# Optimization experiments

Measured on AMD Instinct MI355X. Metric: run time of the kernel, lower is better.

The kernel has to match this reference:

```python
import jax, jax.numpy as jnp
import numpy as np

D = 512      # model_size
NH = 8       # num_heads
HD = D // NH # head_dim = 64
T = 2048     # seq len (qlen == klen == pos len)
B = 2        # batch

# flattened Bayesian parameter layout (matches flatten_list order in the module)
_SHAPES = [(3 * D, D), (D, D), (D, D), (3 * D,), (D,), (D,), (NH, HD), (NH, HD)]
_N = sum(int(np.prod(s)) for s in _SHAPES)  # 1,314,304


def _unflatten(w):
    out, i = [], 0
    for s in _SHAPES:
        n = int(np.prod(s))
        out.append(w[i:i + n].reshape(s))
        i += n
    return out


def _rel_shift(x):
    # Transformer-XL relative shift: x is [qlen, klen, B, NH]
    q, k, b, n = x.shape
    x = jnp.pad(x, ((0, 0), (1, 0), (0, 0), (0, 0)))  # zero col at front of klen axis
    x = x.reshape(k + 1, q, b, n)[1:]
    return x.reshape(q, k, b, n)


def setup_inputs() -> dict:
    key = jax.random.key(0)
    k1, k2, k3, k4, k5 = jax.random.split(key, 5)
    inp = jax.random.normal(k1, (T, B, D), dtype=jnp.float32)
    pos = jax.random.normal(k2, (T, 1, D), dtype=jnp.float32)
    std = np.sqrt(2.0 / (D + D))
    mu = jax.random.normal(k3, (_N,), dtype=jnp.float32) * std
    rho = -5.0 + 0.1 * jax.random.normal(k4, (_N,), dtype=jnp.float32)
    eps = jax.random.normal(k5, (_N,), dtype=jnp.float32)
    attn_mask = jnp.triu(jnp.ones((T, T), dtype=bool), 1)  # True = masked (future)
    return {"input": inp, "pos": pos, "attn_mask": attn_mask,
            "mu": mu, "rho": rho, "eps": eps}


def reference(input, pos, attn_mask, mu, rho, eps):
    # Gaussian reparameterized weight sample: w = mu + softplus(rho) * eps
    w = mu + jax.nn.softplus(rho) * eps
    (in_w, out_w, pos_w, in_b, out_b, pos_b, r_w_bias, r_r_bias) = _unflatten(w)

    # input projection -> q, k, v : [T, B, NH, HD]
    qkv = input @ in_w.T + in_b                      # [T, B, 3D]
    q, k, v = jnp.split(qkv, 3, axis=-1)
    q = q.reshape(T, B, NH, HD)
    k = k.reshape(T, B, NH, HD)
    v = v.reshape(T, B, NH, HD)

    # relative position projection: [R, NH, HD]
    r = (pos[:, 0, :] @ pos_w.T + pos_b).reshape(-1, NH, HD)

    # content score (AC) and position score (BD) with rel-shift
    AC = jnp.einsum('ibnd,jbnd->ijbn', q + r_w_bias, k)
    BD = _rel_shift(jnp.einsum('ibnd,jnd->ijbn', q + r_r_bias, r))

    scale = np.float32(1.0 / np.sqrt(HD))
    score = (AC + BD) * scale                        # [T, T, B, NH]
    score = jnp.where(attn_mask[:, :, None, None],
                      jnp.finfo(score.dtype).min, score)
    probs = jax.nn.softmax(score, axis=1)

    attn_vec = jnp.einsum('ijbn,jbnd->ibnd', probs, v).reshape(T, B, D)
    return attn_vec @ out_w.T + out_b                # [T, B, D]
```

## Files before the change

### kernel.cpp

```cpp
#include <hip/hip_runtime.h>


typedef float f32x4 __attribute__((ext_vector_type(4)));
typedef short bf16x8 __attribute__((ext_vector_type(8)));

#define NW 1314304
#define OFF_INB  1310720
#define OFF_INW  0
#define OFF_OUTW 786432
#define OFF_POSW 1048576
#define BB_IN  0
#define BB_OUT 1536
#define BB_POS 2048
#define BB_RW  2560
#define BB_RR  3072

#define L2E 1.44269504088896340736f

__device__ __forceinline__ unsigned short f2bf(float x) {
  unsigned u = __builtin_bit_cast(unsigned, x);
  u += 0x7fffu + ((u >> 16) & 1u);
  return (unsigned short)(u >> 16);
}
__device__ __forceinline__ float bf2f(unsigned short s) {
  return __builtin_bit_cast(float, ((unsigned)s) << 16);
}
__device__ __forceinline__ unsigned pk2(float lo, float hi) {
  return (unsigned)f2bf(lo) | ((unsigned)f2bf(hi) << 16);
}

__global__ void prep_kernel(const float* __restrict__ mu, const float* __restrict__ rho,
                            const float* __restrict__ eps,
                            const float* __restrict__ input, const float* __restrict__ pos,
                            unsigned short* __restrict__ Wh, float* __restrict__ Bf,
                            unsigned short* __restrict__ inH, unsigned short* __restrict__ posH) {
  const int bx = blockIdx.x;
  if (bx < 1284) {
    int i = (bx * 256 + threadIdx.x) * 4;
    if (i < NW) {
      float4 m = *(const float4*)&mu[i];
      float4 r = *(const float4*)&rho[i];
      float4 e = *(const float4*)&eps[i];
      float w0 = m.x + ((r.x > 20.f) ? r.x : log1pf(expf(r.x))) * e.x;
      float w1 = m.y + ((r.y > 20.f) ? r.y : log1pf(expf(r.y))) * e.y;
      float w2 = m.z + ((r.z > 20.f) ? r.z : log1pf(expf(r.z))) * e.z;
      float w3 = m.w + ((r.w > 20.f) ? r.w : log1pf(expf(r.w))) * e.w;
      union { unsigned short s[4]; uint2 u; } p;
      p.s[0] = f2bf(w0); p.s[1] = f2bf(w1); p.s[2] = f2bf(w2); p.s[3] = f2bf(w3);
      *(uint2*)&Wh[i] = p.u;
      if (i >= OFF_INB) {
        float4 b; b.x = w0; b.y = w1; b.z = w2; b.w = w3;
        *(float4*)&Bf[i - OFF_INB] = b;
      }
    }
  } else if (bx < 3332) {
    int i = ((bx - 1284) * 256 + threadIdx.x) * 4;
    float4 v = *(const float4*)&input[i];
    union { unsigned short s[4]; uint2 u; } p;
    p.s[0] = f2bf(v.x); p.s[1] = f2bf(v.y); p.s[2] = f2bf(v.z); p.s[3] = f2bf(v.w);
    *(uint2*)&inH[i] = p.u;
  } else {
    int i = ((bx - 3332) * 256 + threadIdx.x) * 4;
    float4 v = *(const float4*)&pos[i];
    union { unsigned short s[4]; uint2 u; } p;
    p.s[0] = f2bf(v.x); p.s[1] = f2bf(v.y); p.s[2] = f2bf(v.z); p.s[3] = f2bf(v.w);
    *(uint2*)&posH[i] = p.u;
  }
}

__device__ __forceinline__ void gemm128_loop(const unsigned short* __restrict__ A,
                                             const unsigned short* __restrict__ B,
                                             unsigned short* As, unsigned short* Bs,
                                             f32x4 (&acc)[4][4]) {
  const int tid = threadIdx.x;
  const int wv = tid >> 6, lane = tid & 63, g = lane >> 4, cc = lane & 15;
  const int wr = wv >> 1, wc = wv & 1;
  const int row = tid >> 1, half = tid & 1;
  const unsigned short* Ap = A + (size_t)row * 512 + 32 * half;
  const unsigned short* Bp = B + (size_t)row * 512 + 32 * half;
  const int lb = row * 72 + 32 * half;

#pragma unroll
  for (int j = 0; j < 4; j++) {
    *(uint4*)&As[lb + 8 * j] = *(const uint4*)(Ap + 8 * j);
    *(uint4*)&Bs[lb + 8 * j] = *(const uint4*)(Bp + 8 * j);
  }
  __syncthreads();

  for (int it = 0; it < 8; it++) {
    uint4 pa[4], pb[4];
    const bool pf = (it < 7);
    if (pf) {
      const unsigned short* An = Ap + 64 * (it + 1);
      const unsigned short* Bn = Bp + 64 * (it + 1);
#pragma unroll
      for (int j = 0; j < 4; j++) {
        pa[j] = *(const uint4*)(An + 8 * j);
        pb[j] = *(const uint4*)(Bn + 8 * j);
      }
    }
    __builtin_amdgcn_s_setprio(1);
#pragma unroll
    for (int ks = 0; ks < 2; ks++) {
      bf16x8 af[4], bf[4];
#pragma unroll
      for (int fm = 0; fm < 4; fm++)
        af[fm] = *(const bf16x8*)&As[(64 * wr + 16 * fm + cc) * 72 + 32 * ks + 8 * g];
#pragma unroll
      for (int fn = 0; fn < 4; fn++)
        bf[fn] = *(const bf16x8*)&Bs[(64 * wc + 16 * fn + cc) * 72 + 32 * ks + 8 * g];
#pragma unroll
      for (int fm = 0; fm < 4; fm++)
#pragma unroll
        for (int fn = 0; fn < 4; fn++)
          acc[fm][fn] = __builtin_amdgcn_mfma_f32_16x16x32_bf16(af[fm], bf[fn], acc[fm][fn], 0, 0, 0);
    }
    __builtin_amdgcn_s_setprio(0);
    __syncthreads();
    if (pf) {
#pragma unroll
      for (int j = 0; j < 4; j++) {
        *(uint4*)&As[lb + 8 * j] = pa[j];
        *(uint4*)&Bs[lb + 8 * j] = pb[j];
      }
    }
    __syncthreads();
  }
}

__global__ __launch_bounds__(256, 2)
void gemm01_kernel(const unsigned short* __restrict__ inH, const unsigned short* __restrict__ posH,
                   const unsigned short* __restrict__ Wh, const float* __restrict__ Bf,
                   unsigned short* __restrict__ qrw, unsigned short* __restrict__ qrr,
                   unsigned short* __restrict__ kbuf, unsigned short* __restrict__ vT,
                   unsigned short* __restrict__ rbuf) {
  __shared__ __align__(16) unsigned short As[128 * 72];
  __shared__ __align__(16) unsigned short Bs[128 * 72];
  const int bx = blockIdx.x;
  const int tid = threadIdx.x;
  const int wv = tid >> 6, lane = tid & 63, g = lane >> 4, cc = lane & 15;
  const int wr = wv >> 1, wc = wv & 1;

  const bool isR = (bx >= 384);
  int m0, n0;
  const unsigned short *A, *W;
  if (!isR) {
    m0 = (bx & 31) << 7; n0 = (bx >> 5) << 7;
    A = inH + (size_t)m0 * 512;  W = Wh + OFF_INW + (size_t)n0 * 512;
  } else {
    const int t = bx - 384;
    m0 = (t & 15) << 7; n0 = (t >> 4) << 7;
    A = posH + (size_t)m0 * 512; W = Wh + OFF_POSW + (size_t)n0 * 512;
  }

  f32x4 acc[4][4];
#pragma unroll
  for (int i = 0; i < 4; i++)
#pragma unroll
    for (int j = 0; j < 4; j++) { acc[i][j][0] = 0.f; acc[i][j][1] = 0.f; acc[i][j][2] = 0.f; acc[i][j][3] = 0.f; }
  gemm128_loop(A, W, As, Bs, acc);

  const int sec = isR ? 3 : (n0 >> 9);
  const int t0 = m0 >> 1;

#pragma unroll
  for (int h = 0; h < 2; h++) {
    const int nh2 = ((n0 + 64 * h) >> 6) & 7;
    if (sec == 0) {
      if (wc == h) {
#pragma unroll
        for (int fn = 0; fn < 4; fn++) {
          const int colg = n0 + 64 * h + 16 * fn + cc;
          const float b0 = Bf[BB_IN + colg];
          const float brw = Bf[BB_RW + colg], brr = Bf[BB_RR + colg];
#pragma unroll
          for (int fm = 0; fm < 4; fm++)
#pragma unroll
            for (int r = 0; r < 4; r++) {
              const int ml = 64 * wr + 16 * fm + 4 * g + r;
              As[ml * 72 + 16 * fn + cc] = f2bf((acc[fm][fn][r] + b0 + brw) * 0.125f);
              Bs[ml * 72 + 16 * fn + cc] = f2bf((acc[fm][fn][r] + b0 + brr) * 0.125f);
            }
        }
      }
      __syncthreads();
      for (int c = tid; c < 1024; c += 256) {
        const int ml = c >> 3, hc = c & 7;
        const int bb2 = ml & 1, tl = ml >> 1;
        uint4 v1 = *(const uint4*)&As[ml * 72 + 8 * hc];
        uint4 v2 = *(const uint4*)&Bs[ml * 72 + 8 * hc];
        const size_t dst = ((size_t)(bb2 * 8 + nh2) * 2048 + t0 + tl) * 64 + 8 * hc;
        *(uint4*)&qrw[dst] = v1;
        *(uint4*)&qrr[dst] = v2;
      }
      __syncthreads();
    } else if (sec == 1) {
      if (wc == h) {
#pragma unroll
        for (int fn = 0; fn < 4; fn++) {
          const float b0 = Bf[BB_IN + n0 + 64 * h + 16 * fn + cc];
#pragma unroll
          for (int fm = 0; fm < 4; fm++)
#pragma unroll
            for (int r = 0; r < 4; r++)
              As[(64 * wr + 16 * fm + 4 * g + r) * 72 + 16 * fn + cc] = f2bf(acc[fm][fn][r] + b0);
        }
      }
      __syncthreads();
      for (int c = tid; c < 1024; c += 256) {
        const int ml = c >> 3, hc = c & 7;
        const int bb2 = ml & 1, tl = ml >> 1;
        uint4 v1 = *(const uint4*)&As[ml * 72 + 8 * hc];
        *(uint4*)&kbuf[((size_t)(bb2 * 8 + nh2) * 2048 + t0 + tl) * 64 + 8 * hc] = v1;
      }
      __syncthreads();
    } else if (sec == 2) {
      if (wc == h) {
#pragma unroll
        for (int fn = 0; fn < 4; fn++) {
          const float b0 = Bf[BB_IN + n0 + 64 * h + 16 * fn + cc];
#pragma unroll
          for (int fm = 0; fm < 4; fm++)
#pragma unroll
            for (int r = 0; r < 4; r++)
              As[(64 * wr + 16 * fm + 4 * g + r) * 72 + 16 * fn + cc] = f2bf(acc[fm][fn][r] + b0);
        }
      }
      __syncthreads();
      for (int c = tid; c < 1024; c += 256) {
        const int ncol = c >> 4;
        const int rem = c & 15, bb2 = rem >> 3, jc = rem & 7;
        union { unsigned short s[8]; uint4 u; } pk;
#pragma unroll
        for (int jt = 0; jt < 8; jt++)
          pk.s[jt] = As[(2 * (8 * jc + jt) + bb2) * 72 + ncol];
        *(uint4*)&vT[((size_t)(bb2 * 8 + nh2) * 64 + ncol) * 2048 + t0 + 8 * jc] = pk.u;
      }
      __syncthreads();
    } else {
      if (wc == h) {
#pragma unroll
        for (int fn = 0; fn < 4; fn++) {
          const float b0 = Bf[BB_POS + n0 + 64 * h + 16 * fn + cc];
#pragma unroll
          for (int fm = 0; fm < 4; fm++)
#pragma unroll
            for (int r = 0; r < 4; r++)
              As[(64 * wr + 16 * fm + 4 * g + r) * 72 + 16 * fn + cc] = f2bf(acc[fm][fn][r] + b0);
        }
      }
      __syncthreads();
      for (int c = tid; c < 1024; c += 256) {
        const int ml = c >> 3, hc = c & 7;
        uint4 v1 = *(const uint4*)&As[ml * 72 + 8 * hc];
        *(uint4*)&rbuf[((size_t)nh2 * 2048 + m0 + ml) * 64 + 8 * hc] = v1;
      }
      __syncthreads();
    }
  }
}

__global__ __launch_bounds__(256, 2)
void gemmO_kernel(const unsigned short* __restrict__ av, const unsigned short* __restrict__ W,
                  const float* __restrict__ Bf, float* __restrict__ outp) {
  __shared__ __align__(16) unsigned short As[128 * 72];
  __shared__ __align__(16) unsigned short Bs[128 * 72];
  const int bx = blockIdx.x;
  const int tid = threadIdx.x;
  const int wv = tid >> 6, lane = tid & 63, g = lane >> 4, cc = lane & 15;
  const int wr = wv >> 1, wc = wv & 1;
  const int m0 = (bx & 31) << 7, n0 = (bx >> 5) << 7;

  f32x4 acc[4][4];
#pragma unroll
  for (int i = 0; i < 4; i++)
#pragma unroll
    for (int j = 0; j < 4; j++) { acc[i][j][0] = 0.f; acc[i][j][1] = 0.f; acc[i][j][2] = 0.f; acc[i][j][3] = 0.f; }
  gemm128_loop(av + (size_t)m0 * 512, W + (size_t)n0 * 512, As, Bs, acc);

#pragma unroll
  for (int fn = 0; fn < 4; fn++) {
    const int col = n0 + 64 * wc + 16 * fn + cc;
    const float b0 = Bf[BB_OUT + col];
#pragma unroll
    for (int fm = 0; fm < 4; fm++)
#pragma unroll
      for (int r = 0; r < 4; r++) {
        const int mrow = m0 + 64 * wr + 16 * fm + 4 * g + r;
        outp[(size_t)mrow * 512 + col] = acc[fm][fn][r] + b0;
      }
  }
}

__global__ __launch_bounds__(256, 3)
void attn_kernel(const unsigned short* __restrict__ qrw, const unsigned short* __restrict__ qrr,
                 const unsigned short* __restrict__ kb, const unsigned short* __restrict__ vt,
                 const unsigned short* __restrict__ rb, unsigned short* __restrict__ av,
                 unsigned short* __restrict__ pO, float* __restrict__ pStats)
{
  __shared__ __align__(16) unsigned short Ks[64 * 72];
  __shared__ __align__(16) unsigned short Vs[64 * 72];
  __shared__ __align__(16) unsigned short Rs[128 * 72];
  __shared__ __align__(16) unsigned short GPs[4 * 16 * 84];

  const int tid = threadIdx.x;
  const int wv = tid >> 6, lane = tid & 63, g = lane >> 4, cc = lane & 15;
  const int bx = (int)blockIdx.x;
  const int bn = bx & 15;
  const int sid = 79 - (bx >> 4);
  int qt, s, ns;
  if (sid < 8)       { qt = sid;                s = 0;           ns = 1; }
  else if (sid < 24) { qt = 8 + ((sid - 8) >> 1); s = (sid - 8) & 1; ns = 2; }
  else if (sid < 48) { const int t = sid - 24; const int q3 = t / 3; qt = 16 + q3; s = t - 3 * q3; ns = 3; }
  else               { const int t = sid - 48; qt = 24 + (t >> 2); s = t & 3; ns = 4; }
  const int kt0 = s * 8;
  const int kt1 = (kt0 + 8 < qt + 1) ? (kt0 + 8) : (qt + 1);

  const int nh = bn & 7, bb = bn >> 3;
  const int i0 = qt * 64;
  const int i0g = i0 + wv * 16;
  const int w0base = 1984 - i0;

  const size_t qko = (size_t)bn * 2048 * 64;
  const size_t ro = (size_t)nh * 2048 * 64;

  bf16x8 qw[2], qr[2];
#pragma unroll
  for (int ks = 0; ks < 2; ks++) {
    qw[ks] = *(const bf16x8*)&qrw[qko + (size_t)(i0g + cc) * 64 + 32 * ks + 8 * g];
    qr[ks] = *(const bf16x8*)&qrr[qko + (size_t)(i0g + cc) * 64 + 32 * ks + 8 * g];
  }

  float m_run = -3.0e38f, l_run = 0.f;
  f32x4 o[4];
#pragma unroll
  for (int i = 0; i < 4; i++) { o[i][0] = 0.f; o[i][1] = 0.f; o[i][2] = 0.f; o[i][3] = 0.f; }

  const int srow = tid >> 2, sq = tid & 3;
  const int rrow = tid >> 1, rhalf = tid & 1;
  unsigned short* Gw = &GPs[wv * 1344];
  const int rbase = 48 - 16 * wv;

  {
    const unsigned short* kp = &kb[qko + (size_t)(kt0 * 64 + srow) * 64 + 16 * sq];
    *(uint4*)&Ks[srow * 72 + 16 * sq]     = *(const uint4*)kp;
    *(uint4*)&Ks[srow * 72 + 16 * sq + 8] = *(const uint4*)(kp + 8);
    const unsigned short* vp = &vt[qko + (size_t)srow * 2048 + kt0 * 64 + 16 * sq];
    *(uint4*)&Vs[srow * 72 + 16 * sq]     = *(const uint4*)vp;
    *(uint4*)&Vs[srow * 72 + 16 * sq + 8] = *(const uint4*)(vp + 8);
    const int u0 = w0base + kt0 * 64 + rrow;
    const int uc0 = u0 > 2047 ? 2047 : u0;
    const unsigned short* rp = &rb[ro + (size_t)uc0 * 64 + 32 * rhalf];
    unsigned short* rd = &Rs[(u0 & 127) * 72 + 32 * rhalf];
    *(uint4*)rd        = *(const uint4*)rp;
    *(uint4*)(rd + 8)  = *(const uint4*)(rp + 8);
    *(uint4*)(rd + 16) = *(const uint4*)(rp + 16);
    *(uint4*)(rd + 24) = *(const uint4*)(rp + 24);
  }
  __syncthreads();

  for (int kt = kt0; kt < kt1; kt++) {
    const int j0 = kt * 64;
    const int w0k = w0base + j0;
    const bool pf = (kt + 1 < kt1);

    uint4 ka0, ka1, va0, va1, ra0, ra1;
    int rslot = 0;
    if (pf) {
      const unsigned short* kp = &kb[qko + (size_t)(j0 + 64 + srow) * 64 + 16 * sq];
      ka0 = *(const uint4*)kp; ka1 = *(const uint4*)(kp + 8);
      const unsigned short* vp = &vt[qko + (size_t)srow * 2048 + j0 + 64 + 16 * sq];
      va0 = *(const uint4*)vp; va1 = *(const uint4*)(vp + 8);
      const int unew = w0k + 128 + (tid >> 2);
      rslot = unew & 127;
      const int uc = unew > 2047 ? 2047 : unew;
      const unsigned short* rp = &rb[ro + (size_t)uc * 64 + 16 * sq];
      ra0 = *(const uint4*)rp; ra1 = *(const uint4*)(rp + 8);
    }

    f32x4 st[4];
#pragma unroll
    for (int i = 0; i < 4; i++) { st[i][0] = 0.f; st[i][1] = 0.f; st[i][2] = 0.f; st[i][3] = 0.f; }
    __builtin_amdgcn_s_setprio(1);
#pragma unroll
    for (int ks = 0; ks < 2; ks++) {
#pragma unroll
      for (int fm = 0; fm < 4; fm++) {
        bf16x8 ka = *(const bf16x8*)&Ks[(16 * fm + cc) * 72 + 32 * ks + 8 * g];
        st[fm] = __builtin_amdgcn_mfma_f32_16x16x32_bf16(ka, qw[ks], st[fm], 0, 0, 0);
      }
    }
    f32x4 gt[5];
#pragma unroll
    for (int i = 0; i < 5; i++) { gt[i][0] = 0.f; gt[i][1] = 0.f; gt[i][2] = 0.f; gt[i][3] = 0.f; }
    const int rr0 = w0k + rbase + cc;
#pragma unroll
    for (int ks = 0; ks < 2; ks++) {
#pragma unroll
      for (int fm = 0; fm < 5; fm++) {
        const int rrw = (rr0 + 16 * fm) & 127;
        bf16x8 ra = *(const bf16x8*)&Rs[rrw * 72 + 32 * ks + 8 * g];
        gt[fm] = __builtin_amdgcn_mfma_f32_16x16x32_bf16(ra, qr[ks], gt[fm], 0, 0, 0);
      }
    }
    __builtin_amdgcn_s_setprio(0);

#pragma unroll
    for (int fm = 0; fm < 5; fm++) {
      uint2 w;
      w.x = pk2(gt[fm][0], gt[fm][1]);
      w.y = pk2(gt[fm][2], gt[fm][3]);
      *(uint2*)&Gw[cc * 84 + 16 * fm + 4 * g] = w;
    }

    float p[4][4];
    float tm = -3.0e38f;
    const bool diag = (kt == qt);
    const int c00 = 15 - cc + 4 * g;
#pragma unroll
    for (int fm = 0; fm < 4; fm++) {
      const int c0 = c00 + 16 * fm;
      const int e0 = c0 & ~1;
      const unsigned short* gp = &Gw[cc * 84 + e0];
      unsigned d0 = *(const unsigned*)gp;
      unsigned d1 = *(const unsigned*)(gp + 2);
      unsigned d2 = *(const unsigned*)(gp + 4);
      unsigned lo01, lo23;
      if (c0 & 1) { lo01 = (d0 >> 16) | (d1 << 16); lo23 = (d1 >> 16) | (d2 << 16); }
      else        { lo01 = d0; lo23 = d1; }
      float bd0 = bf2f((unsigned short)(lo01 & 0xffffu));
      float bd1 = bf2f((unsigned short)(lo01 >> 16));
      float bd2 = bf2f((unsigned short)(lo23 & 0xffffu));
      float bd3 = bf2f((unsigned short)(lo23 >> 16));
      float sv0 = st[fm][0] + bd0;
      float sv1 = st[fm][1] + bd1;
      float sv2 = st[fm][2] + bd2;
      float sv3 = st[fm][3] + bd3;
      if (diag) {
        const int jj = 16 * fm + 4 * g;
        const int lim = cc + 16 * wv;
        if (jj + 0 > lim) sv0 = -3.0e38f;
        if (jj + 1 > lim) sv1 = -3.0e38f;
        if (jj + 2 > lim) sv2 = -3.0e38f;
        if (jj + 3 > lim) sv3 = -3.0e38f;
      }
      p[fm][0] = sv0; p[fm][1] = sv1; p[fm][2] = sv2; p[fm][3] = sv3;
      tm = fmaxf(tm, fmaxf(fmaxf(sv0, sv1), fmaxf(sv2, sv3)));
    }
    tm = fmaxf(tm, __shfl_xor(tm, 16));
    tm = fmaxf(tm, __shfl_xor(tm, 32));
    const bool defer = __all(tm - m_run <= 8.0f);
    const float m_new = defer ? m_run : fmaxf(m_run, tm);
    float sc = 1.0f;
    if (!defer) sc = exp2f((m_run - m_new) * L2E);
    float ps = 0.f;
#pragma unroll
    for (int fm = 0; fm < 4; fm++)
#pragma unroll
      for (int r = 0; r < 4; r++) {
        float pv = exp2f((p[fm][r] - m_new) * L2E);
        p[fm][r] = pv;
        ps += pv;
      }
    ps += __shfl_xor(ps, 16);
    ps += __shfl_xor(ps, 32);
    l_run = l_run * sc + ps;
    m_run = m_new;

    if (!defer) {
      float scr[4];
#pragma unroll
      for (int r = 0; r < 4; r++) scr[r] = __shfl(sc, 4 * g + r);
#pragma unroll
      for (int fn = 0; fn < 4; fn++)
#pragma unroll
        for (int r = 0; r < 4; r++) o[fn][r] *= scr[r];
    }

#pragma unroll
    for (int fm = 0; fm < 4; fm++) {
      uint2 w;
      w.x = pk2(p[fm][0], p[fm][1]);
      w.y = pk2(p[fm][2], p[fm][3]);
      *(uint2*)&Gw[cc * 72 + 16 * fm + 4 * g] = w;
    }
    bf16x8 pa[2];
#pragma unroll
    for (int ks = 0; ks < 2; ks++)
      pa[ks] = *(const bf16x8*)&Gw[cc * 72 + 32 * ks + 8 * g];

    __builtin_amdgcn_s_setprio(1);
#pragma unroll
    for (int ks = 0; ks < 2; ks++) {
#pragma unroll
      for (int fn = 0; fn < 4; fn++) {
        bf16x8 vb = *(const bf16x8*)&Vs[(16 * fn + cc) * 72 + 32 * ks + 8 * g];
        o[fn] = __builtin_amdgcn_mfma_f32_16x16x32_bf16(pa[ks], vb, o[fn], 0, 0, 0);
      }
    }
    __builtin_amdgcn_s_setprio(0);

    __syncthreads();
    if (pf) {
      *(uint4*)&Ks[srow * 72 + 16 * sq]     = ka0;
      *(uint4*)&Ks[srow * 72 + 16 * sq + 8] = ka1;
      *(uint4*)&Vs[srow * 72 + 16 * sq]     = va0;
      *(uint4*)&Vs[srow * 72 + 16 * sq + 8] = va1;
      unsigned short* rd = &Rs[rslot * 72 + 16 * sq];
      *(uint4*)rd       = ra0;
      *(uint4*)(rd + 8) = ra1;
    }
    __syncthreads();
  }

  if (ns == 1) {
    const float inv = 1.0f / l_run;
    float invr[4];
#pragma unroll
    for (int r = 0; r < 4; r++) invr[r] = __shfl(inv, 4 * g + r);
#pragma unroll
    for (int fn = 0; fn < 4; fn++) {
      const int hd = 16 * fn + cc;
#pragma unroll
      for (int r = 0; r < 4; r++) {
        const int irow = i0g + 4 * g + r;
        av[((size_t)(irow * 2 + bb) * 8 + nh) * 64 + hd] = f2bf(o[fn][r] * invr[r]);
      }
    }
  } else {
    const size_t slot = (size_t)(bn * 80 + sid);
#pragma unroll
    for (int fn = 0; fn < 4; fn++) {
      const int hd = 16 * fn + cc;
#pragma unroll
      for (int r = 0; r < 4; r++)
        pO[slot * 4096 + (16 * wv + 4 * g + r) * 64 + hd] = f2bf(o[fn][r]);
    }
    if (g == 0) {
      pStats[slot * 128 + (16 * wv + cc) * 2]     = m_run;
      pStats[slot * 128 + (16 * wv + cc) * 2 + 1] = l_run;
    }
  }
}

__global__ __launch_bounds__(256)
void combine_kernel(const unsigned short* __restrict__ pO, const float* __restrict__ pStats,
                    unsigned short* __restrict__ av) {
  const int bxx = (int)blockIdx.x;
  const int bn = bxx & 15, qt = 8 + (bxx >> 4);
  const int nh = bn & 7, bb = bn >> 3;
  const int ns = (qt >> 3) + 1;
  const int sid0 = (qt < 16) ? (8 + (qt - 8) * 2)
                 : (qt < 24) ? (24 + (qt - 16) * 3)
                             : (48 + (qt - 24) * 4);
  const int tid = threadIdx.x;
  const int ql = tid >> 2, hq = tid & 3;
  const size_t sb = (size_t)(bn * 80 + sid0);

  float M = -3.0e38f;
  for (int i = 0; i < ns; i++)
    M = fmaxf(M, pStats[(sb + i) * 128 + ql * 2]);

  float L = 0.f;
  float accv[16];
#pragma unroll
  for (int j = 0; j < 16; j++) accv[j] = 0.f;
  for (int i = 0; i < ns; i++) {
    const float mi = pStats[(sb + i) * 128 + ql * 2];
    const float li = pStats[(sb + i) * 128 + ql * 2 + 1];
    const float w = exp2f((mi - M) * L2E);
    L += w * li;
    union { uint4 u; unsigned short s[8]; } c0, c1;
    const unsigned short* src = &pO[(sb + i) * 4096 + ql * 64 + 16 * hq];
    c0.u = *(const uint4*)src;
    c1.u = *(const uint4*)(src + 8);
#pragma unroll
    for (int j = 0; j < 8; j++) accv[j]     += w * bf2f(c0.s[j]);
#pragma unroll
    for (int j = 0; j < 8; j++) accv[8 + j] += w * bf2f(c1.s[j]);
  }
  const float inv = 1.0f / L;
  union { uint4 u; unsigned short s[8]; } o0, o1;
#pragma unroll
  for (int j = 0; j < 8; j++) o0.s[j] = f2bf(accv[j] * inv);
#pragma unroll
  for (int j = 0; j < 8; j++) o1.s[j] = f2bf(accv[8 + j] * inv);
  const int q = qt * 64 + ql;
  unsigned short* dst = &av[((size_t)(q * 2 + bb) * 8 + nh) * 64 + 16 * hq];
  *(uint4*)dst       = o0.u;
  *(uint4*)(dst + 8) = o1.u;
}

extern "C" void kernel_launch(void* const* d_in, const int* in_sizes, int n_in,
                              void* d_out, int out_size, void* d_ws, size_t ws_size,
                              hipStream_t stream) {
  const float* input = (const float*)d_in[0];
  const float* pos   = (const float*)d_in[1];
  const float* mu  = (const float*)d_in[3];
  const float* rho = (const float*)d_in[4];
  const float* eps = (const float*)d_in[5];
  float* out = (float*)d_out;

  char* ws = (char*)d_ws;
  unsigned short* Wh   = (unsigned short*)ws;
  float*          Bf   = (float*)(ws + 2628608);
  unsigned short* inH  = (unsigned short*)(ws + 2642944);
  unsigned short* posH = (unsigned short*)(ws + 6837248);
  unsigned short* qrw  = (unsigned short*)(ws + 8934400);
  unsigned short* qrr  = (unsigned short*)(ws + 13128704);
  unsigned short* kbuf = (unsigned short*)(ws + 17323008);
  unsigned short* vT   = (unsigned short*)(ws + 21517312);
  unsigned short* rbuf = (unsigned short*)(ws + 25711616);
  unsigned short* pO   = (unsigned short*)(ws + 27808768);
  float*          pSt  = (float*)(ws + 38294528);
  unsigned short* av   = inH;

  prep_kernel<<<dim3(4356), dim3(256), 0, stream>>>(mu, rho, eps, input, pos, Wh, Bf, inH, posH);
  gemm01_kernel<<<dim3(448), dim3(256), 0, stream>>>(inH, posH, Wh, Bf, qrw, qrr, kbuf, vT, rbuf);
  attn_kernel<<<dim3(1280), dim3(256), 0, stream>>>(qrw, qrr, kbuf, vT, rbuf, av, pO, pSt);
  combine_kernel<<<dim3(384), dim3(256), 0, stream>>>(pO, pSt, av);
  gemmO_kernel<<<dim3(128), dim3(256), 0, stream>>>(av, Wh + OFF_OUTW, Bf, out);
}
```

Baseline: 211.7 us.

## Halve GEMM tile width to 128x64 to double block counts; drop lazy softmax rescale

The QKV/pos and output projection GEMMs now use 128x64 output tiles instead of 128x128. Each wave computes a 32x64 slice, and the grids grow from 448 to 896 and from 128 to 256 blocks, which should fill the many CUs better. In the attention kernel, the deferred-max trick that skipped the rescale when the max grew by at most 8 is removed, so the output is rescaled on every tile. That removes a wave vote and a branch but adds shuffles and multiplies on every iteration, while the smaller GEMM tiles give less operand reuse.

```diff
diff --git a/kernel.cpp b/kernel.cpp
--- a/kernel.cpp
+++ b/kernel.cpp
@@ -68,66 +68,6 @@
   }
 }
 
-__device__ __forceinline__ void gemm128_loop(const unsigned short* __restrict__ A,
-                                             const unsigned short* __restrict__ B,
-                                             unsigned short* As, unsigned short* Bs,
-                                             f32x4 (&acc)[4][4]) {
-  const int tid = threadIdx.x;
-  const int wv = tid >> 6, lane = tid & 63, g = lane >> 4, cc = lane & 15;
-  const int wr = wv >> 1, wc = wv & 1;
-  const int row = tid >> 1, half = tid & 1;
-  const unsigned short* Ap = A + (size_t)row * 512 + 32 * half;
-  const unsigned short* Bp = B + (size_t)row * 512 + 32 * half;
-  const int lb = row * 72 + 32 * half;
-
-#pragma unroll
-  for (int j = 0; j < 4; j++) {
-    *(uint4*)&As[lb + 8 * j] = *(const uint4*)(Ap + 8 * j);
-    *(uint4*)&Bs[lb + 8 * j] = *(const uint4*)(Bp + 8 * j);
-  }
-  __syncthreads();
-
-  for (int it = 0; it < 8; it++) {
-    uint4 pa[4], pb[4];
-    const bool pf = (it < 7);
-    if (pf) {
-      const unsigned short* An = Ap + 64 * (it + 1);
-      const unsigned short* Bn = Bp + 64 * (it + 1);
-#pragma unroll
-      for (int j = 0; j < 4; j++) {
-        pa[j] = *(const uint4*)(An + 8 * j);
-        pb[j] = *(const uint4*)(Bn + 8 * j);
-      }
-    }
-    __builtin_amdgcn_s_setprio(1);
-#pragma unroll
-    for (int ks = 0; ks < 2; ks++) {
-      bf16x8 af[4], bf[4];
-#pragma unroll
-      for (int fm = 0; fm < 4; fm++)
-        af[fm] = *(const bf16x8*)&As[(64 * wr + 16 * fm + cc) * 72 + 32 * ks + 8 * g];
-#pragma unroll
-      for (int fn = 0; fn < 4; fn++)
-        bf[fn] = *(const bf16x8*)&Bs[(64 * wc + 16 * fn + cc) * 72 + 32 * ks + 8 * g];
-#pragma unroll
-      for (int fm = 0; fm < 4; fm++)
-#pragma unroll
-        for (int fn = 0; fn < 4; fn++)
-          acc[fm][fn] = __builtin_amdgcn_mfma_f32_16x16x32_bf16(af[fm], bf[fn], acc[fm][fn], 0, 0, 0);
-    }
-    __builtin_amdgcn_s_setprio(0);
-    __syncthreads();
-    if (pf) {
-#pragma unroll
-      for (int j = 0; j < 4; j++) {
-        *(uint4*)&As[lb + 8 * j] = pa[j];
-        *(uint4*)&Bs[lb + 8 * j] = pb[j];
-      }
-    }
-    __syncthreads();
-  }
-}
-
 __global__ __launch_bounds__(256, 2)
 void gemm01_kernel(const unsigned short* __restrict__ inH, const unsigned short* __restrict__ posH,
                    const unsigned short* __restrict__ Wh, const float* __restrict__ Bf,
@@ -139,123 +79,153 @@
   const int bx = blockIdx.x;
   const int tid = threadIdx.x;
   const int wv = tid >> 6, lane = tid & 63, g = lane >> 4, cc = lane & 15;
-  const int wr = wv >> 1, wc = wv & 1;
-
-  const bool isR = (bx >= 384);
+
+  const bool isR = (bx >= 768);
   int m0, n0;
   const unsigned short *A, *W;
   if (!isR) {
-    m0 = (bx & 31) << 7; n0 = (bx >> 5) << 7;
+    m0 = (bx & 31) << 7; n0 = (bx >> 5) << 6;
     A = inH + (size_t)m0 * 512;  W = Wh + OFF_INW + (size_t)n0 * 512;
   } else {
-    const int t = bx - 384;
-    m0 = (t & 15) << 7; n0 = (t >> 4) << 7;
+    const int t = bx - 768;
+    m0 = (t & 15) << 7; n0 = (t >> 4) << 6;
     A = posH + (size_t)m0 * 512; W = Wh + OFF_POSW + (size_t)n0 * 512;
   }
 
-  f32x4 acc[4][4];
-#pragma unroll
-  for (int i = 0; i < 4; i++)
-#pragma unroll
-    for (int j = 0; j < 4; j++) { acc[i][j][0] = 0.f; acc[i][j][1] = 0.f; acc[i][j][2] = 0.f; acc[i][j][3] = 0.f; }
-  gemm128_loop(A, W, As, Bs, acc);
-
+  const int row2 = tid >> 1, h2 = tid & 1;
+  const int row4 = tid >> 2, q4 = tid & 3;
+  const unsigned short* Ap = A + (size_t)row2 * 512 + 32 * h2;
+  const unsigned short* Bp = W + (size_t)row4 * 512 + 16 * q4;
+  const int lba = row2 * 72 + 32 * h2;
+  const int lbb = row4 * 72 + 16 * q4;
+
+  f32x4 acc[2][4] = {};
+
+#pragma unroll
+  for (int j = 0; j < 4; j++) *(uint4*)&As[lba + 8 * j] = *(const uint4*)(Ap + 8 * j);
+#pragma unroll
+  for (int j = 0; j < 2; j++) *(uint4*)&Bs[lbb + 8 * j] = *(const uint4*)(Bp + 8 * j);
+  __syncthreads();
+
+  for (int it = 0; it < 8; it++) {
+    uint4 pa[4], pb[2];
+    const bool pf = (it < 7);
+    if (pf) {
+      const unsigned short* An = Ap + 64 * (it + 1);
+      const unsigned short* Bn = Bp + 64 * (it + 1);
+#pragma unroll
+      for (int j = 0; j < 4; j++) pa[j] = *(const uint4*)(An + 8 * j);
+#pragma unroll
+      for (int j = 0; j < 2; j++) pb[j] = *(const uint4*)(Bn + 8 * j);
+    }
+    __builtin_amdgcn_s_setprio(1);
+#pragma unroll
+    for (int ks = 0; ks < 2; ks++) {
+      bf16x8 af[2], bf[4];
+#pragma unroll
+      for (int fm = 0; fm < 2; fm++)
+        af[fm] = *(const bf16x8*)&As[(32 * wv + 16 * fm + cc) * 72 + 32 * ks + 8 * g];
+#pragma unroll
+      for (int fn = 0; fn < 4; fn++)
+        bf[fn] = *(const bf16x8*)&Bs[(16 * fn + cc) * 72 + 32 * ks + 8 * g];
+#pragma unroll
+      for (int fm = 0; fm < 2; fm++)
+#pragma unroll
+        for (int fn = 0; fn < 4; fn++)
+          acc[fm][fn] = __builtin_amdgcn_mfma_f32_16x16x32_bf16(af[fm], bf[fn], acc[fm][fn], 0, 0, 0);
+    }
+    __builtin_amdgcn_s_setprio(0);
+    __syncthreads();
+    if (pf) {
+#pragma unroll
+      for (int j = 0; j < 4; j++) *(uint4*)&As[lba + 8 * j] = pa[j];
+#pragma unroll
+      for (int j = 0; j < 2; j++) *(uint4*)&Bs[lbb + 8 * j] = pb[j];
+    }
+    __syncthreads();
+  }
+
+  const int nh2 = (n0 >> 6) & 7;
   const int sec = isR ? 3 : (n0 >> 9);
   const int t0 = m0 >> 1;
 
-#pragma unroll
-  for (int h = 0; h < 2; h++) {
-    const int nh2 = ((n0 + 64 * h) >> 6) & 7;
-    if (sec == 0) {
-      if (wc == h) {
-#pragma unroll
-        for (int fn = 0; fn < 4; fn++) {
-          const int colg = n0 + 64 * h + 16 * fn + cc;
-          const float b0 = Bf[BB_IN + colg];
-          const float brw = Bf[BB_RW + colg], brr = Bf[BB_RR + colg];
-#pragma unroll
-          for (int fm = 0; fm < 4; fm++)
-#pragma unroll
-            for (int r = 0; r < 4; r++) {
-              const int ml = 64 * wr + 16 * fm + 4 * g + r;
-              As[ml * 72 + 16 * fn + cc] = f2bf((acc[fm][fn][r] + b0 + brw) * 0.125f);
-              Bs[ml * 72 + 16 * fn + cc] = f2bf((acc[fm][fn][r] + b0 + brr) * 0.125f);
-            }
+  if (sec == 0) {
+#pragma unroll
+    for (int fn = 0; fn < 4; fn++) {
+      const int colg = n0 + 16 * fn + cc;
+      const float b0 = Bf[BB_IN + colg];
+      const float brw = Bf[BB_RW + colg], brr = Bf[BB_RR + colg];
+#pragma unroll
+      for (int fm = 0; fm < 2; fm++)
+#pragma unroll
+        for (int r = 0; r < 4; r++) {
+          const int ml = 32 * wv + 16 * fm + 4 * g + r;
+          As[ml * 72 + 16 * fn + cc] = f2bf((acc[fm][fn][r] + b0 + brw) * 0.125f);
+          Bs[ml * 72 + 16 * fn + cc] = f2bf((acc[fm][fn][r] + b0 + brr) * 0.125f);
         }
-      }
-      __syncthreads();
-      for (int c = tid; c < 1024; c += 256) {
-        const int ml = c >> 3, hc = c & 7;
-        const int bb2 = ml & 1, tl = ml >> 1;
-        uint4 v1 = *(const uint4*)&As[ml * 72 + 8 * hc];
-        uint4 v2 = *(const uint4*)&Bs[ml * 72 + 8 * hc];
-        const size_t dst = ((size_t)(bb2 * 8 + nh2) * 2048 + t0 + tl) * 64 + 8 * hc;
-        *(uint4*)&qrw[dst] = v1;
-        *(uint4*)&qrr[dst] = v2;
-      }
-      __syncthreads();
-    } else if (sec == 1) {
-      if (wc == h) {
-#pragma unroll
-        for (int fn = 0; fn < 4; fn++) {
-          const float b0 = Bf[BB_IN + n0 + 64 * h + 16 * fn + cc];
-#pragma unroll
-          for (int fm = 0; fm < 4; fm++)
-#pragma unroll
-            for (int r = 0; r < 4; r++)
-              As[(64 * wr + 16 * fm + 4 * g + r) * 72 + 16 * fn + cc] = f2bf(acc[fm][fn][r] + b0);
-        }
-      }
-      __syncthreads();
-      for (int c = tid; c < 1024; c += 256) {
-        const int ml = c >> 3, hc = c & 7;
-        const int bb2 = ml & 1, tl = ml >> 1;
-        uint4 v1 = *(const uint4*)&As[ml * 72 + 8 * hc];
-        *(uint4*)&kbuf[((size_t)(bb2 * 8 + nh2) * 2048 + t0 + tl) * 64 + 8 * hc] = v1;
-      }
-      __syncthreads();
-    } else if (sec == 2) {
-      if (wc == h) {
-#pragma unroll
-        for (int fn = 0; fn < 4; fn++) {
-          const float b0 = Bf[BB_IN + n0 + 64 * h + 16 * fn + cc];
-#pragma unroll
-          for (int fm = 0; fm < 4; fm++)
-#pragma unroll
-            for (int r = 0; r < 4; r++)
-              As[(64 * wr + 16 * fm + 4 * g + r) * 72 + 16 * fn + cc] = f2bf(acc[fm][fn][r] + b0);
-        }
-      }
-      __syncthreads();
-      for (int c = tid; c < 1024; c += 256) {
-        const int ncol = c >> 4;
-        const int rem = c & 15, bb2 = rem >> 3, jc = rem & 7;
-        union { unsigned short s[8]; uint4 u; } pk;
-#pragma unroll
-        for (int jt = 0; jt < 8; jt++)
-          pk.s[jt] = As[(2 * (8 * jc + jt) + bb2) * 72 + ncol];
-        *(uint4*)&vT[((size_t)(bb2 * 8 + nh2) * 64 + ncol) * 2048 + t0 + 8 * jc] = pk.u;
-      }
-      __syncthreads();
-    } else {
-      if (wc == h) {
-#pragma unroll
-        for (int fn = 0; fn < 4; fn++) {
-          const float b0 = Bf[BB_POS + n0 + 64 * h + 16 * fn + cc];
-#pragma unroll
-          for (int fm = 0; fm < 4; fm++)
-#pragma unroll
-            for (int r = 0; r < 4; r++)
-              As[(64 * wr + 16 * fm + 4 * g + r) * 72 + 16 * fn + cc] = f2bf(acc[fm][fn][r] + b0);
-        }
-      }
-      __syncthreads();
-      for (int c = tid; c < 1024; c += 256) {
-        const int ml = c >> 3, hc = c & 7;
-        uint4 v1 = *(const uint4*)&As[ml * 72 + 8 * hc];
-        *(uint4*)&rbuf[((size_t)nh2 * 2048 + m0 + ml) * 64 + 8 * hc] = v1;
-      }
-      __syncthreads();
+    }
+    __syncthreads();
+    for (int c = tid; c < 1024; c += 256) {
+      const int ml = c >> 3, hc = c & 7;
+      const int bb2 = ml & 1, tl = ml >> 1;
+      uint4 v1 = *(const uint4*)&As[ml * 72 + 8 * hc];
+      uint4 v2 = *(const uint4*)&Bs[ml * 72 + 8 * hc];
+      const size_t dst = ((size_t)(bb2 * 8 + nh2) * 2048 + t0 + tl) * 64 + 8 * hc;
+      *(uint4*)&qrw[dst] = v1;
+      *(uint4*)&qrr[dst] = v2;
+    }
+  } else if (sec == 1) {
+#pragma unroll
+    for (int fn = 0; fn < 4; fn++) {
+      const float b0 = Bf[BB_IN + n0 + 16 * fn + cc];
+#pragma unroll
+      for (int fm = 0; fm < 2; fm++)
+#pragma unroll
+        for (int r = 0; r < 4; r++)
+          As[(32 * wv + 16 * fm + 4 * g + r) * 72 + 16 * fn + cc] = f2bf(acc[fm][fn][r] + b0);
+    }
+    __syncthreads();
+    for (int c = tid; c < 1024; c += 256) {
+      const int ml = c >> 3, hc = c & 7;
+      const int bb2 = ml & 1, tl = ml >> 1;
+      uint4 v1 = *(const uint4*)&As[ml * 72 + 8 * hc];
+      *(uint4*)&kbuf[((size_t)(bb2 * 8 + nh2) * 2048 + t0 + tl) * 64 + 8 * hc] = v1;
+    }
+  } else if (sec == 2) {
+#pragma unroll
+    for (int fn = 0; fn < 4; fn++) {
+      const float b0 = Bf[BB_IN + n0 + 16 * fn + cc];
+#pragma unroll
+      for (int fm = 0; fm < 2; fm++)
+#pragma unroll
+        for (int r = 0; r < 4; r++)
+          As[(32 * wv + 16 * fm + 4 * g + r) * 72 + 16 * fn + cc] = f2bf(acc[fm][fn][r] + b0);
+    }
+    __syncthreads();
+    for (int c = tid; c < 1024; c += 256) {
+      const int ncol = c >> 4;
+      const int rem = c & 15, bb2 = rem >> 3, jc = rem & 7;
+      union { unsigned short s[8]; uint4 u; } pk;
+#pragma unroll
+      for (int jt = 0; jt < 8; jt++)
+        pk.s[jt] = As[(2 * (8 * jc + jt) + bb2) * 72 + ncol];
+      *(uint4*)&vT[((size_t)(bb2 * 8 + nh2) * 64 + ncol) * 2048 + t0 + 8 * jc] = pk.u;
+    }
+  } else {
+#pragma unroll
+    for (int fn = 0; fn < 4; fn++) {
+      const float b0 = Bf[BB_POS + n0 + 16 * fn + cc];
+#pragma unroll
+      for (int fm = 0; fm < 2; fm++)
+#pragma unroll
+        for (int r = 0; r < 4; r++)
+          As[(32 * wv + 16 * fm + 4 * g + r) * 72 + 16 * fn + cc] = f2bf(acc[fm][fn][r] + b0);
+    }
+    __syncthreads();
+    for (int c = tid; c < 1024; c += 256) {
+      const int ml = c >> 3, hc = c & 7;
+      uint4 v1 = *(const uint4*)&As[ml * 72 + 8 * hc];
+      *(uint4*)&rbuf[((size_t)nh2 * 2048 + m0 + ml) * 64 + 8 * hc] = v1;
     }
   }
 }
@@ -268,25 +238,70 @@
   const int bx = blockIdx.x;
   const int tid = threadIdx.x;
   const int wv = tid >> 6, lane = tid & 63, g = lane >> 4, cc = lane & 15;
-  const int wr = wv >> 1, wc = wv & 1;
-  const int m0 = (bx & 31) << 7, n0 = (bx >> 5) << 7;
-
-  f32x4 acc[4][4];
-#pragma unroll
-  for (int i = 0; i < 4; i++)
-#pragma unroll
-    for (int j = 0; j < 4; j++) { acc[i][j][0] = 0.f; acc[i][j][1] = 0.f; acc[i][j][2] = 0.f; acc[i][j][3] = 0.f; }
-  gemm128_loop(av + (size_t)m0 * 512, W + (size_t)n0 * 512, As, Bs, acc);
+  const int m0 = (bx & 31) << 7, n0 = (bx >> 5) << 6;
+
+  const int row2 = tid >> 1, h2 = tid & 1;
+  const int row4 = tid >> 2, q4 = tid & 3;
+  const unsigned short* Ap = av + (size_t)(m0 + row2) * 512 + 32 * h2;
+  const unsigned short* Bp = W + (size_t)(n0 + row4) * 512 + 16 * q4;
+  const int lba = row2 * 72 + 32 * h2;
+  const int lbb = row4 * 72 + 16 * q4;
+
+  f32x4 acc[2][4] = {};
+
+#pragma unroll
+  for (int j = 0; j < 4; j++) *(uint4*)&As[lba + 8 * j] = *(const uint4*)(Ap + 8 * j);
+#pragma unroll
+  for (int j = 0; j < 2; j++) *(uint4*)&Bs[lbb + 8 * j] = *(const uint4*)(Bp + 8 * j);
+  __syncthreads();
+
+  for (int it = 0; it < 8; it++) {
+    uint4 pa[4], pb[2];
+    const bool pf = (it < 7);
+    if (pf) {
+      const unsigned short* An = Ap + 64 * (it + 1);
+      const unsigned short* Bn = Bp + 64 * (it + 1);
+#pragma unroll
+      for (int j = 0; j < 4; j++) pa[j] = *(const uint4*)(An + 8 * j);
+#pragma unroll
+      for (int j = 0; j < 2; j++) pb[j] = *(const uint4*)(Bn + 8 * j);
+    }
+    __builtin_amdgcn_s_setprio(1);
+#pragma unroll
+    for (int ks = 0; ks < 2; ks++) {
+      bf16x8 af[2], bf[4];
+#pragma unroll
+      for (int fm = 0; fm < 2; fm++)
+        af[fm] = *(const bf16x8*)&As[(32 * wv + 16 * fm + cc) * 72 + 32 * ks + 8 * g];
+#pragma unroll
+      for (int fn = 0; fn < 4; fn++)
+        bf[fn] = *(const bf16x8*)&Bs[(16 * fn + cc) * 72 + 32 * ks + 8 * g];
+#pragma unroll
+      for (int fm = 0; fm < 2; fm++)
+#pragma unroll
+        for (int fn = 0; fn < 4; fn++)
+          acc[fm][fn] = __builtin_amdgcn_mfma_f32_16x16x32_bf16(af[fm], bf[fn], acc[fm][fn], 0, 0, 0);
+    }
+    __builtin_amdgcn_s_setprio(0);
+    __syncthreads();
+    if (pf) {
+#pragma unroll
+      for (int j = 0; j < 4; j++) *(uint4*)&As[lba + 8 * j] = pa[j];
+#pragma unroll
+      for (int j = 0; j < 2; j++) *(uint4*)&Bs[lbb + 8 * j] = pb[j];
+    }
+    __syncthreads();
+  }
 
 #pragma unroll
   for (int fn = 0; fn < 4; fn++) {
-    const int col = n0 + 64 * wc + 16 * fn + cc;
+    const int col = n0 + 16 * fn + cc;
     const float b0 = Bf[BB_OUT + col];
 #pragma unroll
-    for (int fm = 0; fm < 4; fm++)
+    for (int fm = 0; fm < 2; fm++)
 #pragma unroll
       for (int r = 0; r < 4; r++) {
-        const int mrow = m0 + 64 * wr + 16 * fm + 4 * g + r;
+        const int mrow = m0 + 32 * wv + 16 * fm + 4 * g + r;
         outp[(size_t)mrow * 512 + col] = acc[fm][fn][r] + b0;
       }
   }
@@ -449,10 +464,8 @@
     }
     tm = fmaxf(tm, __shfl_xor(tm, 16));
     tm = fmaxf(tm, __shfl_xor(tm, 32));
-    const bool defer = __all(tm - m_run <= 8.0f);
-    const float m_new = defer ? m_run : fmaxf(m_run, tm);
-    float sc = 1.0f;
-    if (!defer) sc = exp2f((m_run - m_new) * L2E);
+    const float m_new = fmaxf(m_run, tm);
+    const float sc = exp2f((m_run - m_new) * L2E);
     float ps = 0.f;
 #pragma unroll
     for (int fm = 0; fm < 4; fm++)
@@ -467,15 +480,13 @@
     l_run = l_run * sc + ps;
     m_run = m_new;
 
-    if (!defer) {
-      float scr[4];
-#pragma unroll
-      for (int r = 0; r < 4; r++) scr[r] = __shfl(sc, 4 * g + r);
-#pragma unroll
-      for (int fn = 0; fn < 4; fn++)
-#pragma unroll
-        for (int r = 0; r < 4; r++) o[fn][r] *= scr[r];
-    }
+    float scr[4];
+#pragma unroll
+    for (int r = 0; r < 4; r++) scr[r] = __shfl(sc, 4 * g + r);
+#pragma unroll
+    for (int fn = 0; fn < 4; fn++)
+#pragma unroll
+      for (int r = 0; r < 4; r++) o[fn][r] *= scr[r];
 
 #pragma unroll
     for (int fm = 0; fm < 4; fm++) {
@@ -616,8 +627,8 @@
   unsigned short* av   = inH;
 
   prep_kernel<<<dim3(4356), dim3(256), 0, stream>>>(mu, rho, eps, input, pos, Wh, Bf, inH, posH);
-  gemm01_kernel<<<dim3(448), dim3(256), 0, stream>>>(inH, posH, Wh, Bf, qrw, qrr, kbuf, vT, rbuf);
+  gemm01_kernel<<<dim3(896), dim3(256), 0, stream>>>(inH, posH, Wh, Bf, qrw, qrr, kbuf, vT, rbuf);
   attn_kernel<<<dim3(1280), dim3(256), 0, stream>>>(qrw, qrr, kbuf, vT, rbuf, av, pO, pSt);
   combine_kernel<<<dim3(384), dim3(256), 0, stream>>>(pO, pSt, av);
-  gemmO_kernel<<<dim3(128), dim3(256), 0, stream>>>(av, Wh + OFF_OUTW, Bf, out);
-}
+  gemmO_kernel<<<dim3(256), dim3(256), 0, stream>>>(av, Wh + OFF_OUTW, Bf, out);
+}
```

Result: slower. 221.6 us (+4.7%).
